# Optimization experiments

Measured on AMD Instinct MI355X. Metric: run time of the kernel, lower is better.

Reference implementation:

```python
import jax, jax.numpy as jnp
import numpy as np

D_MODEL = 1024
N_HEADS = 16
D_K = D_MODEL // N_HEADS


def setup_inputs() -> dict:
    key = jax.random.key(0)
    ks = jax.random.split(key, 12)
    B, S = 2, 2048
    scale = 1.0 / np.sqrt(D_MODEL)
    inp = {
        "q": jax.random.normal(ks[0], (B, S, D_MODEL), jnp.float32),
        "k": jax.random.normal(ks[1], (B, S, D_MODEL), jnp.float32),
        "v": jax.random.normal(ks[2], (B, S, D_MODEL), jnp.float32),
        "k_pe": jax.random.normal(ks[3], (N_HEADS, D_K, S), jnp.float32),
        "Wq": jax.random.normal(ks[4], (D_MODEL, D_MODEL), jnp.float32) * scale,
        "bq": jnp.zeros((D_MODEL,), jnp.float32),
        "Wk": jax.random.normal(ks[5], (D_MODEL, D_MODEL), jnp.float32) * scale,
        "bk": jnp.zeros((D_MODEL,), jnp.float32),
        "Wv": jax.random.normal(ks[6], (D_MODEL, D_MODEL), jnp.float32) * scale,
        "bv": jnp.zeros((D_MODEL,), jnp.float32),
        "Wo": jax.random.normal(ks[7], (D_MODEL, D_MODEL), jnp.float32) * scale,
        "bo": jnp.zeros((D_MODEL,), jnp.float32),
    }
    return inp


def reference(q, k, v, k_pe, Wq, bq, Wk, bk, Wv, bv, Wo, bo):
    B, S, _ = q.shape
    # projections -> [B, H, S, d_k]
    def split_heads(x):
        return x.reshape(B, S, N_HEADS, D_K).transpose(0, 2, 1, 3)
    qh = split_heads(q @ Wq + bq)
    kh = split_heads(k @ Wk + bk)
    vh = split_heads(v @ Wv + bv)
    # content scores + relative positional scores (two matmuls, summed)
    scores = jnp.einsum("bhsd,bhtd->bhst", qh, kh)
    scores = scores + jnp.einsum("bhsd,hdt->bhst", qh, k_pe)
    scores = scores / jnp.sqrt(jnp.asarray(D_K, qh.dtype))
    attn = jax.nn.softmax(scores, axis=-1)
    out = jnp.einsum("bhst,bhtd->bhsd", attn, vh)  # [B,H,S,d_k]
    out = out.transpose(0, 2, 1, 3).reshape(B, S, D_MODEL)
    return out @ Wo + bo
```

## Files before the change

kernel.cpp:

```cpp
#include <hip/hip_runtime.h>
#include <stdint.h>
#include <math.h>

typedef __bf16 bf16;
typedef __attribute__((ext_vector_type(8))) __bf16 bf16x8;
typedef __attribute__((ext_vector_type(4))) __bf16 bf16x4;
typedef __attribute__((ext_vector_type(4))) float f32x4;

#define MFMA_BF16(a, b, c) __builtin_amdgcn_mfma_f32_16x16x32_bf16((a), (b), (c), 0, 0, 0)

#if __has_builtin(__builtin_amdgcn_exp2f)
#define EXP2F __builtin_amdgcn_exp2f
#else
#define EXP2F exp2f
#endif

#define QSCALE 0.18033688011112042f

__device__ __forceinline__ void gl_lds16(const bf16* g, bf16* l) {
  __builtin_amdgcn_global_load_lds(
      (__attribute__((address_space(1))) unsigned int*)(uintptr_t)(g),
      (__attribute__((address_space(3))) unsigned int*)(l),
      16, 0, 0);
}

__global__ __launch_bounds__(256) void prep(
    const float* __restrict__ q, const float* __restrict__ k,
    const float* __restrict__ v, bf16* __restrict__ qb,
    bf16* __restrict__ kb, bf16* __restrict__ vb,
    const float* __restrict__ W0, const float* __restrict__ W1,
    const float* __restrict__ W2, const float* __restrict__ W3,
    bf16* __restrict__ Wt)
{
  __shared__ float tile[64][65];
  const int tid = threadIdx.x;
  const int bid = blockIdx.x;
  if (bid < 6144) {
    const int z = bid >> 11;
    const int idx = bid & 2047;
    const float* s = (z == 0) ? q : (z == 1) ? k : v;
    bf16* d = (z == 0) ? qb : (z == 1) ? kb : vb;
    size_t i = ((size_t)idx * 256 + tid) * 8;
    float4 a = *(const float4*)(s + i);
    float4 b = *(const float4*)(s + i + 4);
    bf16x8 o;
    o[0] = (bf16)a.x; o[1] = (bf16)a.y; o[2] = (bf16)a.z; o[3] = (bf16)a.w;
    o[4] = (bf16)b.x; o[5] = (bf16)b.y; o[6] = (bf16)b.z; o[7] = (bf16)b.w;
    *(bf16x8*)(d + i) = o;
  } else {
    const int t = bid - 6144;
    const int z = t >> 8;
    const int rem = t & 255;
    const int r0 = (rem >> 4) * 64, c0 = (rem & 15) * 64;
    const float* src = (z == 0) ? W0 : (z == 1) ? W1 : (z == 2) ? W2 : W3;
    bf16* dst = Wt + (size_t)z * (1024 * 1024);
#pragma unroll
    for (int h = 0; h < 2; ++h) {
      int qq = tid + h * 256;
      int row = qq >> 3, cc = qq & 7;
      float4 a = *(const float4*)(src + (size_t)(r0 + row) * 1024 + c0 + cc * 8);
      float4 b = *(const float4*)(src + (size_t)(r0 + row) * 1024 + c0 + cc * 8 + 4);
      tile[row][cc * 8 + 0] = a.x; tile[row][cc * 8 + 1] = a.y;
      tile[row][cc * 8 + 2] = a.z; tile[row][cc * 8 + 3] = a.w;
      tile[row][cc * 8 + 4] = b.x; tile[row][cc * 8 + 5] = b.y;
      tile[row][cc * 8 + 6] = b.z; tile[row][cc * 8 + 7] = b.w;
    }
    __syncthreads();
#pragma unroll
    for (int h = 0; h < 2; ++h) {
      int qq = tid + h * 256;
      int row = qq >> 3, cc = qq & 7;
      bf16x8 o;
#pragma unroll
      for (int e = 0; e < 8; ++e) o[e] = (bf16)tile[cc * 8 + e][row];
      *(bf16x8*)(dst + (size_t)(c0 + row) * 1024 + r0 + cc * 8) = o;
    }
  }
}

template <int MODE>
__device__ __forceinline__ void gemm_body(
    const bf16* __restrict__ A, const bf16* __restrict__ Wt,
    const float* __restrict__ bias, float oscale,
    const float* __restrict__ kpe, void* __restrict__ out_v)
{
  __shared__ __align__(16) bf16 As[128 * 32];
  __shared__ __align__(16) bf16 Bs[128 * 32];
  const int tid = threadIdx.x;
  const int w = tid >> 6, lane = tid & 63;
  const int lm = lane & 15, quad = lane >> 4;
  const int wr = w >> 1, wc = w & 1;
  const int m0 = blockIdx.y * 128, n0 = blockIdx.x * 128;

  f32x4 zero4 = {0.f, 0.f, 0.f, 0.f};
  f32x4 acc[4][4];
#pragma unroll
  for (int i = 0; i < 4; ++i)
#pragma unroll
    for (int j = 0; j < 4; ++j) acc[i][j] = zero4;

  for (int kb = 0; kb < 32; ++kb) {
    __syncthreads();
#pragma unroll
    for (int h = 0; h < 2; ++h) {
      int qq = tid + h * 256;
      int row = qq >> 2, cs = qq & 3;
      int cc = cs ^ ((row >> 1) & 3);
      gl_lds16(A + (size_t)(m0 + row) * 1024 + kb * 32 + cc * 8, As + qq * 8);
      gl_lds16(Wt + (size_t)(n0 + row) * 1024 + kb * 32 + cc * 8, Bs + qq * 8);
    }
    __syncthreads();

    bf16x8 af[4], bfv[4];
#pragma unroll
    for (int i = 0; i < 4; ++i) {
      int row = wr * 64 + i * 16 + lm;
      af[i] = *(const bf16x8*)(As + row * 32 + ((quad ^ ((row >> 1) & 3)) * 8));
    }
#pragma unroll
    for (int j = 0; j < 4; ++j) {
      int row = wc * 64 + j * 16 + lm;
      bfv[j] = *(const bf16x8*)(Bs + row * 32 + ((quad ^ ((row >> 1) & 3)) * 8));
    }
#pragma unroll
    for (int i = 0; i < 4; ++i)
#pragma unroll
      for (int j = 0; j < 4; ++j)
        acc[i][j] = MFMA_BF16(af[i], bfv[j], acc[i][j]);
  }

  const int ncol = n0 + wc * 64;
  float bv4[4];
#pragma unroll
  for (int j = 0; j < 4; ++j) bv4[j] = bias[ncol + j * 16 + lm];
#pragma unroll
  for (int i = 0; i < 4; ++i) {
    const int mbase = m0 + wr * 64 + i * 16 + quad * 4;
    const int b = mbase >> 11, s = mbase & 2047;
#pragma unroll
    for (int j = 0; j < 4; ++j) {
      const int ng = ncol + j * 16 + lm;
      const int hh = ng >> 6, d = ng & 63;
      if (MODE == 2) {
        bf16x4 o;
#pragma unroll
        for (int r = 0; r < 4; ++r) o[r] = (bf16)(acc[i][j][r] + bv4[j]);
        *(bf16x4*)((bf16*)out_v + ((size_t)(b * 16 + hh) * 64 + d) * 2048 + s) = o;
      } else if (MODE == 1) {
        float4 p4 = *(const float4*)(kpe + ((size_t)(hh * 64 + d)) * 2048 + s);
        float pe[4] = {p4.x, p4.y, p4.z, p4.w};
#pragma unroll
        for (int r = 0; r < 4; ++r) {
          float val = acc[i][j][r] + bv4[j] + pe[r];
          ((bf16*)out_v)[(((size_t)(b * 16 + hh)) * 2048 + (s + r)) * 64 + d] =
              (bf16)val;
        }
      } else if (MODE == 0) {
#pragma unroll
        for (int r = 0; r < 4; ++r) {
          float val = acc[i][j][r] + bv4[j];
          ((bf16*)out_v)[(((size_t)(b * 16 + hh)) * 2048 + (s + r)) * 64 + d] =
              (bf16)(val * oscale);
        }
      } else {
#pragma unroll
        for (int r = 0; r < 4; ++r) {
          float val = acc[i][j][r] + bv4[j];
          ((float*)out_v)[(size_t)(mbase + r) * 1024 + ng] = val;
        }
      }
    }
  }
}

__global__ __launch_bounds__(256) void qkv_gemm(
    const bf16* __restrict__ qb, const bf16* __restrict__ kb, const bf16* __restrict__ vb,
    const bf16* __restrict__ Wt, const float* __restrict__ biq,
    const float* __restrict__ bik, const float* __restrict__ biv,
    const float* __restrict__ kpe,
    bf16* __restrict__ Qs, bf16* __restrict__ Ks, bf16* __restrict__ Vts)
{
  const int z = blockIdx.z;
  if (z == 0) {
    gemm_body<0>(qb, Wt, biq, QSCALE, nullptr, Qs);
  } else if (z == 1) {
    gemm_body<1>(kb, Wt + (size_t)1 * 1024 * 1024, bik, 1.f, kpe, Ks);
  } else {
    gemm_body<2>(vb, Wt + (size_t)2 * 1024 * 1024, biv, 1.f, nullptr, Vts);
  }
}

__global__ __launch_bounds__(256) void out_gemm(
    const bf16* __restrict__ A, const bf16* __restrict__ Wt,
    const float* __restrict__ bias, float* __restrict__ out)
{
  gemm_body<3>(A, Wt, bias, 1.f, nullptr, out);
}

__global__ __launch_bounds__(512) void flash_attn(
    const bf16* __restrict__ Q, const bf16* __restrict__ K,
    const bf16* __restrict__ Vt, bf16* __restrict__ O)
{
  __shared__ __align__(16) bf16 Qt[128 * 64];
  __shared__ __align__(16) bf16 Kt[2][64 * 64];
  __shared__ __align__(16) bf16 Vs[2][64 * 64];
  __shared__ __align__(16) bf16 Ps[128 * 72];

  const int tid = threadIdx.x;
  const int w = tid >> 6, lane = tid & 63;
  const int lm = lane & 15, quad = lane >> 4;
  const int bh = blockIdx.y;
  const int s0 = blockIdx.x * 128;
  const size_t qkbase = (size_t)bh * (2048 * 64);
  const size_t vbase = (size_t)bh * (64 * 2048);

#pragma unroll
  for (int h = 0; h < 2; ++h) {
    int qq = tid + h * 512;
    int row = qq >> 3, cs = qq & 7;
    int cc = cs ^ (row & 7);
    gl_lds16(Q + qkbase + (size_t)(s0 + row) * 64 + cc * 8, Qt + qq * 8);
  }
  {
    int row = tid >> 3, cs = tid & 7;
    int cc = cs ^ (row & 7);
    gl_lds16(K + qkbase + (size_t)row * 64 + cc * 8, Kt[0] + tid * 8);
    gl_lds16(Vt + vbase + (size_t)row * 2048 + cc * 8, Vs[0] + tid * 8);
  }
  __syncthreads();

  bf16x8 qa0, qa1;
  {
    int row = w * 16 + lm;
    qa0 = *(const bf16x8*)(Qt + row * 64 + ((quad ^ (row & 7)) * 8));
    qa1 = *(const bf16x8*)(Qt + row * 64 + (((quad + 4) ^ (row & 7)) * 8));
  }

  f32x4 zero4 = {0.f, 0.f, 0.f, 0.f};
  float l_part = 0.f;
  f32x4 oacc[4];
#pragma unroll
  for (int dt = 0; dt < 4; ++dt) oacc[dt] = zero4;

  const int prow = (w * 16 + lm) * 72;

  for (int kt = 0; kt < 32; ++kt) {
    const int cur = kt & 1;
    if (kt < 31) {
      const int t1 = (kt + 1) * 64;
      int row = tid >> 3, cs = tid & 7;
      int cc = cs ^ (row & 7);
      gl_lds16(K + qkbase + (size_t)(t1 + row) * 64 + cc * 8, Kt[cur ^ 1] + tid * 8);
      gl_lds16(Vt + vbase + (size_t)row * 2048 + t1 + cc * 8, Vs[cur ^ 1] + tid * 8);
    }

#pragma unroll
    for (int c = 0; c < 4; ++c) {
      int row = c * 16 + lm;
      bf16x8 kb0 = *(const bf16x8*)(Kt[cur] + row * 64 + ((quad ^ (row & 7)) * 8));
      bf16x8 kb1 = *(const bf16x8*)(Kt[cur] + row * 64 + (((quad + 4) ^ (row & 7)) * 8));
      f32x4 z = MFMA_BF16(kb0, qa0, zero4);
      f32x4 st = MFMA_BF16(kb1, qa1, z);
      bf16x4 pk;
#pragma unroll
      for (int r = 0; r < 4; ++r) {
        float p = EXP2F(st[r]);
        l_part += p;
        pk[r] = (bf16)p;
      }
      *(bf16x4*)(Ps + prow + c * 16 + quad * 4) = pk;
    }

    bf16x8 pa0 = *(const bf16x8*)(Ps + prow + quad * 8);
    bf16x8 pa1 = *(const bf16x8*)(Ps + prow + 32 + quad * 8);
#pragma unroll
    for (int dt = 0; dt < 4; ++dt) {
      int row = dt * 16 + lm;
      bf16x8 va0 = *(const bf16x8*)(Vs[cur] + row * 64 + ((quad ^ (row & 7)) * 8));
      bf16x8 va1 = *(const bf16x8*)(Vs[cur] + row * 64 + (((quad + 4) ^ (row & 7)) * 8));
      oacc[dt] = MFMA_BF16(va0, pa0, oacc[dt]);
      oacc[dt] = MFMA_BF16(va1, pa1, oacc[dt]);
    }

    __syncthreads();
  }

  float l = l_part;
  l += __shfl_xor(l, 16, 64);
  l += __shfl_xor(l, 32, 64);
  float inv = 1.f / l;
#pragma unroll
  for (int dt = 0; dt < 4; ++dt)
#pragma unroll
    for (int r = 0; r < 4; ++r)
      Ps[prow + dt * 16 + quad * 4 + r] = (bf16)(oacc[dt][r] * inv);

  const int b = bh >> 4, hh = bh & 15;
  const int srow = s0 + w * 16 + lm;
  const size_t ob = ((size_t)(b * 2048 + srow)) * 1024 + hh * 64;
#pragma unroll
  for (int half = 0; half < 2; ++half) {
    bf16x8 ov = *(const bf16x8*)(Ps + prow + (half * 4 + quad) * 8);
    *(bf16x8*)(O + ob + (half * 4 + quad) * 8) = ov;
  }
}

extern "C" void kernel_launch(void* const* d_in, const int* in_sizes, int n_in,
                              void* d_out, int out_size, void* d_ws, size_t ws_size,
                              hipStream_t stream) {
  (void)in_sizes; (void)n_in; (void)out_size; (void)ws_size;
  const float* q   = (const float*)d_in[0];
  const float* k   = (const float*)d_in[1];
  const float* v   = (const float*)d_in[2];
  const float* kpe = (const float*)d_in[3];
  const float* Wq  = (const float*)d_in[4];
  const float* bq  = (const float*)d_in[5];
  const float* Wk  = (const float*)d_in[6];
  const float* bk  = (const float*)d_in[7];
  const float* Wv  = (const float*)d_in[8];
  const float* bv  = (const float*)d_in[9];
  const float* Wo  = (const float*)d_in[10];
  const float* bo  = (const float*)d_in[11];

  const size_t NT = 4u * 1024 * 1024;
  bf16* ws  = (bf16*)d_ws;
  bf16* Wt  = ws;
  bf16* qb  = Wt + NT;
  bf16* kb  = qb + NT;
  bf16* vb  = kb + NT;
  bf16* Qs  = vb + NT;
  bf16* Ks  = Qs + NT;
  bf16* Vts = Ks + NT;
  bf16* Oa  = Vts + NT;

  prep<<<dim3(7168), 256, 0, stream>>>(q, k, v, qb, kb, vb, Wq, Wk, Wv, Wo, Wt);
  qkv_gemm<<<dim3(8, 32, 3), 256, 0, stream>>>(qb, kb, vb, Wt, bq, bk, bv, kpe,
                                               Qs, Ks, Vts);
  flash_attn<<<dim3(16, 32), 512, 0, stream>>>(Qs, Ks, Vts, Oa);
  out_gemm<<<dim3(8, 32), 256, 0, stream>>>(Oa, Wt + 3u * 1024 * 1024, bo,
                                            (float*)d_out);
}
```

Baseline: 248.2 us.

## Double-buffer GEMM LDS tiles and pre-convert k_pe to bf16 in prep

The shared GEMM body now uses two LDS buffers so the global-to-LDS loads for the next K-slice are issued before the MFMAs on the current slice, with one barrier per iteration instead of two. The k_pe positional tensor is converted to bf16 in the prep kernel, reusing the attention-output workspace buffer, so the K-projection epilogue reads half the bytes. The cost is double the LDS per GEMM block, which may reduce occupancy, plus an extra conversion pass, and k_pe is rounded to bf16 before it is added.

```diff
diff --git a/kernel.cpp b/kernel.cpp
--- a/kernel.cpp
+++ b/kernel.cpp
@@ -30,7 +30,8 @@
     bf16* __restrict__ kb, bf16* __restrict__ vb,
     const float* __restrict__ W0, const float* __restrict__ W1,
     const float* __restrict__ W2, const float* __restrict__ W3,
-    bf16* __restrict__ Wt)
+    bf16* __restrict__ Wt,
+    const float* __restrict__ kpe, bf16* __restrict__ kpeb)
 {
   __shared__ float tile[64][65];
   const int tid = threadIdx.x;
@@ -47,7 +48,7 @@
     o[0] = (bf16)a.x; o[1] = (bf16)a.y; o[2] = (bf16)a.z; o[3] = (bf16)a.w;
     o[4] = (bf16)b.x; o[5] = (bf16)b.y; o[6] = (bf16)b.z; o[7] = (bf16)b.w;
     *(bf16x8*)(d + i) = o;
-  } else {
+  } else if (bid < 7168) {
     const int t = bid - 6144;
     const int z = t >> 8;
     const int rem = t & 255;
@@ -75,6 +76,15 @@
       for (int e = 0; e < 8; ++e) o[e] = (bf16)tile[cc * 8 + e][row];
       *(bf16x8*)(dst + (size_t)(c0 + row) * 1024 + r0 + cc * 8) = o;
     }
+  } else {
+    const int idx = bid - 7168;
+    size_t i = ((size_t)idx * 256 + tid) * 8;
+    float4 a = *(const float4*)(kpe + i);
+    float4 b = *(const float4*)(kpe + i + 4);
+    bf16x8 o;
+    o[0] = (bf16)a.x; o[1] = (bf16)a.y; o[2] = (bf16)a.z; o[3] = (bf16)a.w;
+    o[4] = (bf16)b.x; o[5] = (bf16)b.y; o[6] = (bf16)b.z; o[7] = (bf16)b.w;
+    *(bf16x8*)(kpeb + i) = o;
   }
 }
 
@@ -82,10 +92,9 @@
 __device__ __forceinline__ void gemm_body(
     const bf16* __restrict__ A, const bf16* __restrict__ Wt,
     const float* __restrict__ bias, float oscale,
-    const float* __restrict__ kpe, void* __restrict__ out_v)
-{
-  __shared__ __align__(16) bf16 As[128 * 32];
-  __shared__ __align__(16) bf16 Bs[128 * 32];
+    const bf16* __restrict__ kpeb, void* __restrict__ out_v,
+    bf16* __restrict__ As, bf16* __restrict__ Bs)
+{
   const int tid = threadIdx.x;
   const int w = tid >> 6, lane = tid & 63;
   const int lm = lane & 15, quad = lane >> 4;
@@ -99,34 +108,47 @@
 #pragma unroll
     for (int j = 0; j < 4; ++j) acc[i][j] = zero4;
 
-  for (int kb = 0; kb < 32; ++kb) {
-    __syncthreads();
+  auto stage = [&](int buf, int kb) {
 #pragma unroll
     for (int h = 0; h < 2; ++h) {
       int qq = tid + h * 256;
       int row = qq >> 2, cs = qq & 3;
       int cc = cs ^ ((row >> 1) & 3);
-      gl_lds16(A + (size_t)(m0 + row) * 1024 + kb * 32 + cc * 8, As + qq * 8);
-      gl_lds16(Wt + (size_t)(n0 + row) * 1024 + kb * 32 + cc * 8, Bs + qq * 8);
-    }
-    __syncthreads();
-
+      gl_lds16(A + (size_t)(m0 + row) * 1024 + kb * 32 + cc * 8,
+               As + buf * 4096 + qq * 8);
+      gl_lds16(Wt + (size_t)(n0 + row) * 1024 + kb * 32 + cc * 8,
+               Bs + buf * 4096 + qq * 8);
+    }
+  };
+
+  stage(0, 0);
+  __syncthreads();
+
+  int cur = 0;
+  for (int kb = 0; kb < 32; ++kb) {
+    if (kb < 31) stage(cur ^ 1, kb + 1);
+
+    const bf16* Ab = As + cur * 4096;
+    const bf16* Bb = Bs + cur * 4096;
     bf16x8 af[4], bfv[4];
 #pragma unroll
     for (int i = 0; i < 4; ++i) {
       int row = wr * 64 + i * 16 + lm;
-      af[i] = *(const bf16x8*)(As + row * 32 + ((quad ^ ((row >> 1) & 3)) * 8));
+      af[i] = *(const bf16x8*)(Ab + row * 32 + ((quad ^ ((row >> 1) & 3)) * 8));
     }
 #pragma unroll
     for (int j = 0; j < 4; ++j) {
       int row = wc * 64 + j * 16 + lm;
-      bfv[j] = *(const bf16x8*)(Bs + row * 32 + ((quad ^ ((row >> 1) & 3)) * 8));
+      bfv[j] = *(const bf16x8*)(Bb + row * 32 + ((quad ^ ((row >> 1) & 3)) * 8));
     }
 #pragma unroll
     for (int i = 0; i < 4; ++i)
 #pragma unroll
       for (int j = 0; j < 4; ++j)
         acc[i][j] = MFMA_BF16(af[i], bfv[j], acc[i][j]);
+
+    __syncthreads();
+    cur ^= 1;
   }
 
   const int ncol = n0 + wc * 64;
@@ -147,11 +169,10 @@
         for (int r = 0; r < 4; ++r) o[r] = (bf16)(acc[i][j][r] + bv4[j]);
         *(bf16x4*)((bf16*)out_v + ((size_t)(b * 16 + hh) * 64 + d) * 2048 + s) = o;
       } else if (MODE == 1) {
-        float4 p4 = *(const float4*)(kpe + ((size_t)(hh * 64 + d)) * 2048 + s);
-        float pe[4] = {p4.x, p4.y, p4.z, p4.w};
+        bf16x4 p4 = *(const bf16x4*)(kpeb + ((size_t)(hh * 64 + d)) * 2048 + s);
 #pragma unroll
         for (int r = 0; r < 4; ++r) {
-          float val = acc[i][j][r] + bv4[j] + pe[r];
+          float val = acc[i][j][r] + bv4[j] + (float)p4[r];
           ((bf16*)out_v)[(((size_t)(b * 16 + hh)) * 2048 + (s + r)) * 64 + d] =
               (bf16)val;
         }
@@ -177,16 +198,18 @@
     const bf16* __restrict__ qb, const bf16* __restrict__ kb, const bf16* __restrict__ vb,
     const bf16* __restrict__ Wt, const float* __restrict__ biq,
     const float* __restrict__ bik, const float* __restrict__ biv,
-    const float* __restrict__ kpe,
+    const bf16* __restrict__ kpeb,
     bf16* __restrict__ Qs, bf16* __restrict__ Ks, bf16* __restrict__ Vts)
 {
+  __shared__ __align__(16) bf16 As[2 * 128 * 32];
+  __shared__ __align__(16) bf16 Bs[2 * 128 * 32];
   const int z = blockIdx.z;
   if (z == 0) {
-    gemm_body<0>(qb, Wt, biq, QSCALE, nullptr, Qs);
+    gemm_body<0>(qb, Wt, biq, QSCALE, nullptr, Qs, As, Bs);
   } else if (z == 1) {
-    gemm_body<1>(kb, Wt + (size_t)1 * 1024 * 1024, bik, 1.f, kpe, Ks);
+    gemm_body<1>(kb, Wt + (size_t)1 * 1024 * 1024, bik, 1.f, kpeb, Ks, As, Bs);
   } else {
-    gemm_body<2>(vb, Wt + (size_t)2 * 1024 * 1024, biv, 1.f, nullptr, Vts);
+    gemm_body<2>(vb, Wt + (size_t)2 * 1024 * 1024, biv, 1.f, nullptr, Vts, As, Bs);
   }
 }
 
@@ -194,7 +217,9 @@
     const bf16* __restrict__ A, const bf16* __restrict__ Wt,
     const float* __restrict__ bias, float* __restrict__ out)
 {
-  gemm_body<3>(A, Wt, bias, 1.f, nullptr, out);
+  __shared__ __align__(16) bf16 As[2 * 128 * 32];
+  __shared__ __align__(16) bf16 Bs[2 * 128 * 32];
+  gemm_body<3>(A, Wt, bias, 1.f, nullptr, out, As, Bs);
 }
 
 __global__ __launch_bounds__(512) void flash_attn(
@@ -332,9 +357,11 @@
   bf16* Ks  = Qs + NT;
   bf16* Vts = Ks + NT;
   bf16* Oa  = Vts + NT;
-
-  prep<<<dim3(7168), 256, 0, stream>>>(q, k, v, qb, kb, vb, Wq, Wk, Wv, Wo, Wt);
-  qkv_gemm<<<dim3(8, 32, 3), 256, 0, stream>>>(qb, kb, vb, Wt, bq, bk, bv, kpe,
+  bf16* kpeb = Oa;
+
+  prep<<<dim3(8192), 256, 0, stream>>>(q, k, v, qb, kb, vb, Wq, Wk, Wv, Wo, Wt,
+                                       kpe, kpeb);
+  qkv_gemm<<<dim3(8, 32, 3), 256, 0, stream>>>(qb, kb, vb, Wt, bq, bk, bv, kpeb,
                                                Qs, Ks, Vts);
   flash_attn<<<dim3(16, 32), 512, 0, stream>>>(Qs, Ks, Vts, Oa);
   out_gemm<<<dim3(8, 32), 256, 0, stream>>>(Oa, Wt + 3u * 1024 * 1024, bo,
```

Result: no change. 245.7 us (-1.0%).
